# Kernel optimization log

Measured on AMD Instinct MI355X. Metric: run time of the kernel, lower is better.

## Reference

```python
import jax, jax.numpy as jnp
import numpy as np

K = 1024
H = 16

def setup_inputs() -> dict:
    key = jax.random.key(0)
    ks = jax.random.split(key, 6)
    s = 1.0 / np.sqrt(K)
    return {
        "x": jax.random.normal(ks[0], (2, 2048, K), dtype=jnp.float32),
        "Wq": jax.random.uniform(ks[1], (K, K), jnp.float32, -s, s),
        "Wk": jax.random.uniform(ks[2], (K, K), jnp.float32, -s, s),
        "Wv": jax.random.uniform(ks[3], (K, K), jnp.float32, -s, s),
        "Wu": jax.random.uniform(ks[4], (K, K), jnp.float32, -s, s),
        "bu": jax.random.uniform(ks[5], (K,), jnp.float32, -s, s),
    }

def reference(x, Wq, Wk, Wv, Wu, bu):
    b, t, k = x.shape
    hd = k // H  # head dim = 64
    scale = jnp.asarray(k, x.dtype) ** 0.25  # Bloem-style: scale q and k each by k^(1/4)
    # nn.Linear(bias=False): y = x @ W.T
    q = (jnp.einsum('btk,ok->bto', x, Wq) / scale).reshape(b, t, H, hd)
    kk = (jnp.einsum('btk,ok->bto', x, Wk) / scale).reshape(b, t, H, hd)
    v = jnp.einsum('btk,ok->bto', x, Wv).reshape(b, t, H, hd)
    dot = jnp.einsum('bthd,bshd->bhts', q, kk)  # [b,h,t,t]
    att = jax.nn.softmax(dot, axis=-1)
    out = jnp.einsum('bhts,bshd->bthd', att, v).reshape(b, t, k)
    return jnp.einsum('btk,ok->bto', out, Wu) + bu
```

## Files before the change

kernel.cpp:

```cpp
#include <hip/hip_runtime.h>

typedef __bf16 bf16;
typedef bf16  bf16x8 __attribute__((ext_vector_type(8)));
typedef bf16  bf16x4 __attribute__((ext_vector_type(4)));
typedef float f32x4  __attribute__((ext_vector_type(4)));

#define MFMA16(a, b, c) __builtin_amdgcn_mfma_f32_16x16x32_bf16((a), (b), (c), 0, 0, 0)
#define AS1 __attribute__((address_space(1)))
#define AS3 __attribute__((address_space(3)))

__device__ __forceinline__ void gld_lds16(const bf16* g, bf16* l) {
    __builtin_amdgcn_global_load_lds((AS1 void*)(g), (AS3 void*)(l), 16, 0, 0);
}


__global__ __launch_bounds__(256) void cvt_all(const float* __restrict__ x,
                                               const float* __restrict__ Wq, const float* __restrict__ Wk,
                                               const float* __restrict__ Wv, const float* __restrict__ Wu,
                                               bf16* ox, bf16* oq, bf16* ok, bf16* ov, bf16* ou,
                                               float sq, float sk) {
    int bid = blockIdx.x;
    const float* src; bf16* dst; float sc; int base;
    if (bid < 4096) { src = x; dst = ox; sc = 1.0f; base = bid; }
    else {
        int w = (bid - 4096) >> 10; base = (bid - 4096) & 1023;
        switch (w) {
            case 0:  src = Wq; dst = oq; sc = sq;   break;
            case 1:  src = Wk; dst = ok; sc = sk;   break;
            case 2:  src = Wv; dst = ov; sc = 1.0f; break;
            default: src = Wu; dst = ou; sc = 1.0f; break;
        }
    }
    int idx = (base * 256 + threadIdx.x) * 4;
    float4 v = *(const float4*)(src + idx);
    bf16x4 o;
    o[0] = (bf16)(v.x * sc); o[1] = (bf16)(v.y * sc);
    o[2] = (bf16)(v.z * sc); o[3] = (bf16)(v.w * sc);
    *(bf16x4*)(dst + idx) = o;
}

__device__ __forceinline__ void gemm_core(const bf16* __restrict__ A, const bf16* __restrict__ B,
                                          int mBase, int nBase, bf16* As, bf16* Bs,
                                          f32x4 acc[4][4]) {
    const int tid = threadIdx.x;
    const int wave = tid >> 6, lane = tid & 63;
    const int g = lane >> 4, lr = lane & 15;
    const int wm = (wave & 1) << 6, wn = (wave >> 1) << 6;
    const int q = lane >> 2;
    const int cswz = ((lane & 3) ^ ((lane >> 3) & 3)) << 3;
    const int pcs  = (g ^ ((lr >> 1) & 3)) << 3;

    const int rb0 = wave << 4, rb1 = rb0 + 64;
    const bf16* a0 = A + (size_t)(mBase + rb0 + q) * 1024 + cswz;
    const bf16* a1 = A + (size_t)(mBase + rb1 + q) * 1024 + cswz;
    const bf16* b0 = B + (size_t)(nBase + rb0 + q) * 1024 + cswz;
    const bf16* b1 = B + (size_t)(nBase + rb1 + q) * 1024 + cswz;

    for (int k0 = 0; k0 < 1024; k0 += 32) {
        __syncthreads();
        gld_lds16(a0 + k0, As + rb0 * 32);
        gld_lds16(a1 + k0, As + rb1 * 32);
        gld_lds16(b0 + k0, Bs + rb0 * 32);
        gld_lds16(b1 + k0, Bs + rb1 * 32);
        __syncthreads();

        bf16x8 af[4], bfr[4];
#pragma unroll
        for (int i = 0; i < 4; i++)
            af[i] = *(const bf16x8*)&As[(wm + (i << 4) + lr) * 32 + pcs];
#pragma unroll
        for (int j = 0; j < 4; j++)
            bfr[j] = *(const bf16x8*)&Bs[(wn + (j << 4) + lr) * 32 + pcs];
#pragma unroll
        for (int i = 0; i < 4; i++)
#pragma unroll
            for (int j = 0; j < 4; j++)
                acc[i][j] = MFMA16(af[i], bfr[j], acc[i][j]);
    }
}

__global__ __launch_bounds__(256) void gemm_qkv(const bf16* __restrict__ A,
                                                const bf16* __restrict__ Wq, const bf16* __restrict__ Wk,
                                                const bf16* __restrict__ Wv,
                                                bf16* __restrict__ Qo, bf16* __restrict__ Ko,
                                                bf16* __restrict__ Vto) {
    __shared__ bf16 As[128 * 32];
    __shared__ bf16 Bs[128 * 32];
    const int tid = threadIdx.x;
    const int wave = tid >> 6, lane = tid & 63;
    const int g = lane >> 4, lr = lane & 15;
    const int wm = (wave & 1) << 6, wn = (wave >> 1) << 6;
    const int z = blockIdx.z;

    const bf16 *Ap, *Bp;
    int mBase, nBase;
    if (z == 2) { Ap = Wv; Bp = A;            mBase = blockIdx.x * 128; nBase = blockIdx.y * 128; }
    else        { Ap = A;  Bp = z ? Wk : Wq;  mBase = blockIdx.y * 128; nBase = blockIdx.x * 128; }

    f32x4 acc[4][4] = {};
    gemm_core(Ap, Bp, mBase, nBase, As, Bs, acc);

#pragma unroll
    for (int i = 0; i < 4; i++)
#pragma unroll
        for (int j = 0; j < 4; j++)
#pragma unroll
            for (int r = 0; r < 4; r++) {
                int m = mBase + wm + (i << 4) + (g << 2) + r;
                int n = nBase + wn + (j << 4) + lr;
                bf16 v = (bf16)acc[i][j][r];
                if (z == 2) {
                    int h = m >> 6, d = m & 63, b = n >> 11, t = n & 2047;
                    Vto[((size_t)(((b << 4) + h) << 6) + d) * 2048 + t] = v;
                } else {
                    int b = m >> 11, t = m & 2047, h = n >> 6, d = n & 63;
                    bf16* dst = (z == 0) ? Qo : Ko;
                    dst[(((size_t)((b << 4) + h) * 2048 + t) << 6) + d] = v;
                }
            }
}

__global__ __launch_bounds__(256) void gemm_out(const bf16* __restrict__ A, const bf16* __restrict__ B,
                                                const float* __restrict__ bias, float* __restrict__ out) {
    __shared__ bf16 As[128 * 32];
    __shared__ bf16 Bs[128 * 32];
    const int tid = threadIdx.x;
    const int wave = tid >> 6, lane = tid & 63;
    const int g = lane >> 4, lr = lane & 15;
    const int wm = (wave & 1) << 6, wn = (wave >> 1) << 6;
    const int mBase = blockIdx.y * 128, nBase = blockIdx.x * 128;

    f32x4 acc[4][4] = {};
    gemm_core(A, B, mBase, nBase, As, Bs, acc);

#pragma unroll
    for (int i = 0; i < 4; i++)
#pragma unroll
        for (int j = 0; j < 4; j++) {
            int n = nBase + wn + (j << 4) + lr;
            float bv = bias[n];
#pragma unroll
            for (int r = 0; r < 4; r++) {
                int m = mBase + wm + (i << 4) + (g << 2) + r;
                out[((size_t)m << 10) + n] = acc[i][j][r] + bv;
            }
        }
}

__global__ __launch_bounds__(256, 4) void attn(const bf16* __restrict__ Q, const bf16* __restrict__ Kt,
                                               const bf16* __restrict__ Vt, bf16* __restrict__ O) {
    __shared__ bf16 Qs[2][64][32];
    __shared__ bf16 Ks[2][128][32];
    __shared__ bf16 Vs[4][64][32];
    bf16 (*Ps)[16][32] = (bf16(*)[16][32]) & Qs[0][0][0];

    const int tid = threadIdx.x;
    const int wave = tid >> 6, lane = tid & 63;
    const int g = lane >> 4, lr = lane & 15;
    const int q = lane >> 2;
    const int cswz = ((lane & 3) ^ ((lane >> 3) & 3)) << 3;
    const int pcs  = (g ^ ((lr >> 1) & 3)) << 3;
    const int pw0 = ((((g >> 1))     ^ ((lr >> 1) & 3)) << 3) + ((g & 1) << 2);
    const int pw1 = (((2 + (g >> 1)) ^ ((lr >> 1) & 3)) << 3) + ((g & 1) << 2);

    const int bid = blockIdx.x;
    const int bh = ((bid & 7) << 2) | (bid >> 8);
    const int qt = (bid >> 3) & 31;
    const int qBase = qt << 6;

    const bf16* Qg = Q + ((size_t)bh * 2048 + qBase) * 64;
    const bf16* Kg = Kt + (size_t)bh * 2048 * 64;
    const bf16* Vg = Vt + (size_t)bh * 64 * 2048;

#pragma unroll
    for (int i = 0; i < 2; i++) {
        int bi = (wave << 1) + i;
        int p = bi >> 2, rb = (bi & 3) << 4;
        gld_lds16(Qg + (rb + q) * 64 + (p << 5) + cswz, &Qs[p][rb][0]);
    }
    __syncthreads();

    bf16x8 qf[2];
#pragma unroll
    for (int ks = 0; ks < 2; ks++)
        qf[ks] = *(const bf16x8*)&Qs[ks][(wave << 4) + lr][pcs];

    bf16x8 ones;
#pragma unroll
    for (int i = 0; i < 8; i++) ones[i] = (bf16)1.0f;

    f32x4 oacc[4] = {};
    f32x4 oaccL = {};

    for (int s0 = 0; s0 < 2048; s0 += 128) {
        __syncthreads();
#pragma unroll
        for (int i = 0; i < 4; i++) {
            int bi = (wave << 2) + i;
            {
                int p = bi >> 3, rb = (bi & 7) << 4;
                gld_lds16(Kg + (size_t)(s0 + rb + q) * 64 + (p << 5) + cswz, &Ks[p][rb][0]);
            }
            {
                int p = bi >> 2, rb = (bi & 3) << 4;
                gld_lds16(Vg + (size_t)(rb + q) * 2048 + s0 + (p << 5) + cswz, &Vs[p][rb][0]);
            }
        }
        __syncthreads();

#pragma unroll
        for (int ks2 = 0; ks2 < 4; ks2++) {
            f32x4 sacc[2] = {};
#pragma unroll
            for (int isub = 0; isub < 2; isub++) {
                int is = (ks2 << 1) + isub;
#pragma unroll
                for (int ks = 0; ks < 2; ks++) {
                    bf16x8 kf = *(const bf16x8*)&Ks[ks][(is << 4) + lr][pcs];
                    sacc[isub] = MFMA16(kf, qf[ks], sacc[isub]);
                }
            }
#pragma unroll
            for (int isub = 0; isub < 2; isub++) {
                f32x4 s = sacc[isub];
                bf16x4 pb;
                pb[0] = (bf16)__builtin_amdgcn_exp2f(s[0]);
                pb[1] = (bf16)__builtin_amdgcn_exp2f(s[1]);
                pb[2] = (bf16)__builtin_amdgcn_exp2f(s[2]);
                pb[3] = (bf16)__builtin_amdgcn_exp2f(s[3]);
                *(bf16x4*)&Ps[wave][lr][isub ? pw1 : pw0] = pb;
            }
            bf16x8 pf = *(const bf16x8*)&Ps[wave][lr][pcs];
#pragma unroll
            for (int jd = 0; jd < 4; jd++) {
                bf16x8 vf = *(const bf16x8*)&Vs[ks2][(jd << 4) + lr][pcs];
                oacc[jd] = MFMA16(pf, vf, oacc[jd]);
            }
            oaccL = MFMA16(pf, ones, oaccL);
        }
    }

    float linv[4];
#pragma unroll
    for (int r = 0; r < 4; r++) linv[r] = 1.0f / oaccL[r];

    const int b = bh >> 4, h = bh & 15;
#pragma unroll
    for (int jd = 0; jd < 4; jd++)
#pragma unroll
        for (int r = 0; r < 4; r++) {
            int t = qBase + (wave << 4) + (g << 2) + r;
            int col = (h << 6) + (jd << 4) + lr;
            O[(((size_t)(b * 2048 + t)) << 10) + col] = (bf16)(oacc[jd][r] * linv[r]);
        }
}

extern "C" void kernel_launch(void* const* d_in, const int* in_sizes, int n_in,
                              void* d_out, int out_size, void* d_ws, size_t ws_size,
                              hipStream_t stream) {
    const float* x  = (const float*)d_in[0];
    const float* Wq = (const float*)d_in[1];
    const float* Wk = (const float*)d_in[2];
    const float* Wv = (const float*)d_in[3];
    const float* Wu = (const float*)d_in[4];
    const float* bu = (const float*)d_in[5];
    float* out = (float*)d_out;

    char* ws = (char*)d_ws;
    bf16* xbf  = (bf16*)(ws);
    bf16* wqbf = (bf16*)(ws + ((size_t)8  << 20));
    bf16* wkbf = (bf16*)(ws + ((size_t)10 << 20));
    bf16* wvbf = (bf16*)(ws + ((size_t)12 << 20));
    bf16* wubf = (bf16*)(ws + ((size_t)14 << 20));
    bf16* Qb   = (bf16*)(ws + ((size_t)16 << 20));
    bf16* Kb   = (bf16*)(ws + ((size_t)24 << 20));
    bf16* Vtb  = (bf16*)(ws + ((size_t)32 << 20));
    bf16* attnO = xbf;

    const float iscale_k = 0.17677669529663687f;
    const float iscale_q = 0.25503540109f;

    cvt_all<<<8192, 256, 0, stream>>>(x, Wq, Wk, Wv, Wu, xbf, wqbf, wkbf, wvbf, wubf,
                                      iscale_q, iscale_k);

    gemm_qkv<<<dim3(8, 32, 3), 256, 0, stream>>>(xbf, wqbf, wkbf, wvbf, Qb, Kb, Vtb);
    attn<<<dim3(1024), 256, 0, stream>>>(Qb, Kb, Vtb, attnO);
    gemm_out<<<dim3(8, 32), 256, 0, stream>>>(attnO, wubf, bu, out);
}
```

Before: 193.8 us.

## Transpose GEMM operand roles so epilogue stores become 4-element vector writes

Swaps the A/B roles in the QKV and output projections so that each lane's four accumulator rows map to contiguous output elements. This lets the epilogues write bf16x4 and float4 vectors instead of scalar stores, and lets the bias be loaded as float4. Q and K are merged into one weight matrix indexed by the grid y range, which assumes wq and wk sit contiguously in the workspace. Grid shapes change to match, which alters the block traversal order and the cache reuse of X.

```diff
diff --git a/kernel.cpp b/kernel.cpp
--- a/kernel.cpp
+++ b/kernel.cpp
@@ -79,8 +79,8 @@
     }
 }
 
-__global__ __launch_bounds__(256) void gemm_qkv(const bf16* __restrict__ A,
-                                                const bf16* __restrict__ Wq, const bf16* __restrict__ Wk,
+__global__ __launch_bounds__(256) void gemm_qkv(const bf16* __restrict__ X,
+                                                const bf16* __restrict__ Wqk,
                                                 const bf16* __restrict__ Wv,
                                                 bf16* __restrict__ Qo, bf16* __restrict__ Ko,
                                                 bf16* __restrict__ Vto) {
@@ -90,37 +90,53 @@
     const int wave = tid >> 6, lane = tid & 63;
     const int g = lane >> 4, lr = lane & 15;
     const int wm = (wave & 1) << 6, wn = (wave >> 1) << 6;
-    const int z = blockIdx.z;
-
-    const bf16 *Ap, *Bp;
-    int mBase, nBase;
-    if (z == 2) { Ap = Wv; Bp = A;            mBase = blockIdx.x * 128; nBase = blockIdx.y * 128; }
-    else        { Ap = A;  Bp = z ? Wk : Wq;  mBase = blockIdx.y * 128; nBase = blockIdx.x * 128; }
+    const int my = blockIdx.y;
+    const bool qk = (my < 16);
+
+    const bf16* Ap = qk ? Wqk : X;
+    const bf16* Bp = qk ? X   : Wv;
+    const int mBase = qk ? my * 128 : blockIdx.x * 128;
+    const int nBase = qk ? blockIdx.x * 128 : (my - 16) * 128;
 
     f32x4 acc[4][4] = {};
     gemm_core(Ap, Bp, mBase, nBase, As, Bs, acc);
 
-#pragma unroll
-    for (int i = 0; i < 4; i++)
-#pragma unroll
-        for (int j = 0; j < 4; j++)
-#pragma unroll
-            for (int r = 0; r < 4; r++) {
-                int m = mBase + wm + (i << 4) + (g << 2) + r;
-                int n = nBase + wn + (j << 4) + lr;
-                bf16 v = (bf16)acc[i][j][r];
-                if (z == 2) {
-                    int h = m >> 6, d = m & 63, b = n >> 11, t = n & 2047;
-                    Vto[((size_t)(((b << 4) + h) << 6) + d) * 2048 + t] = v;
-                } else {
-                    int b = m >> 11, t = m & 2047, h = n >> 6, d = n & 63;
-                    bf16* dst = (z == 0) ? Qo : Ko;
-                    dst[(((size_t)((b << 4) + h) * 2048 + t) << 6) + d] = v;
-                }
-            }
-}
-
-__global__ __launch_bounds__(256) void gemm_out(const bf16* __restrict__ A, const bf16* __restrict__ B,
+    if (qk) {
+#pragma unroll
+        for (int i = 0; i < 4; i++) {
+            int m0 = mBase + wm + (i << 4) + (g << 2);
+            bf16* dst = (m0 >> 10) ? Ko : Qo;
+            int feat = m0 & 1023;
+            int h = feat >> 6, d = feat & 63;
+#pragma unroll
+            for (int j = 0; j < 4; j++) {
+                int t = nBase + wn + (j << 4) + lr;
+                int b = t >> 11, tl = t & 2047;
+                bf16x4 v;
+#pragma unroll
+                for (int r = 0; r < 4; r++) v[r] = (bf16)acc[i][j][r];
+                *(bf16x4*)&dst[(((size_t)((b << 4) + h) * 2048 + tl) << 6) + d] = v;
+            }
+        }
+    } else {
+#pragma unroll
+        for (int i = 0; i < 4; i++) {
+            int t0 = mBase + wm + (i << 4) + (g << 2);
+            int b = t0 >> 11, tl = t0 & 2047;
+#pragma unroll
+            for (int j = 0; j < 4; j++) {
+                int o = nBase + wn + (j << 4) + lr;
+                int h = o >> 6, d = o & 63;
+                bf16x4 v;
+#pragma unroll
+                for (int r = 0; r < 4; r++) v[r] = (bf16)acc[i][j][r];
+                *(bf16x4*)&Vto[((size_t)(((b << 4) + h) << 6) + d) * 2048 + tl] = v;
+            }
+        }
+    }
+}
+
+__global__ __launch_bounds__(256) void gemm_out(const bf16* __restrict__ Wu, const bf16* __restrict__ A,
                                                 const float* __restrict__ bias, float* __restrict__ out) {
     __shared__ bf16 As[128 * 32];
     __shared__ bf16 Bs[128 * 32];
@@ -131,20 +147,23 @@
     const int mBase = blockIdx.y * 128, nBase = blockIdx.x * 128;
 
     f32x4 acc[4][4] = {};
-    gemm_core(A, B, mBase, nBase, As, Bs, acc);
-
-#pragma unroll
-    for (int i = 0; i < 4; i++)
+    gemm_core(Wu, A, mBase, nBase, As, Bs, acc);
+
+#pragma unroll
+    for (int i = 0; i < 4; i++) {
+        int o = mBase + wm + (i << 4) + (g << 2);
+        float4 bv = *(const float4*)&bias[o];
 #pragma unroll
         for (int j = 0; j < 4; j++) {
-            int n = nBase + wn + (j << 4) + lr;
-            float bv = bias[n];
-#pragma unroll
-            for (int r = 0; r < 4; r++) {
-                int m = mBase + wm + (i << 4) + (g << 2) + r;
-                out[((size_t)m << 10) + n] = acc[i][j][r] + bv;
-            }
-        }
+            int t = nBase + wn + (j << 4) + lr;
+            float4 v;
+            v.x = acc[i][j][0] + bv.x;
+            v.y = acc[i][j][1] + bv.y;
+            v.z = acc[i][j][2] + bv.z;
+            v.w = acc[i][j][3] + bv.w;
+            *(float4*)&out[((size_t)t << 10) + o] = v;
+        }
+    }
 }
 
 __global__ __launch_bounds__(256, 4) void attn(const bf16* __restrict__ Q, const bf16* __restrict__ Kt,
@@ -283,7 +302,7 @@
     cvt_all<<<8192, 256, 0, stream>>>(x, Wq, Wk, Wv, Wu, xbf, wqbf, wkbf, wvbf, wubf,
                                       iscale_q, iscale_k);
 
-    gemm_qkv<<<dim3(8, 32, 3), 256, 0, stream>>>(xbf, wqbf, wkbf, wvbf, Qb, Kb, Vtb);
+    gemm_qkv<<<dim3(32, 24), 256, 0, stream>>>(xbf, wqbf, wvbf, Qb, Kb, Vtb);
     attn<<<dim3(1024), 256, 0, stream>>>(Qb, Kb, Vtb, attnO);
-    gemm_out<<<dim3(8, 32), 256, 0, stream>>>(attnO, wubf, bu, out);
-}
+    gemm_out<<<dim3(32, 8), 256, 0, stream>>>(wubf, attnO, bu, out);
+}
```

After: 190.6 us. About the same (-1.7%).
